# Performance work log

Measured on AMD Instinct MI355X. Metric: run time of the kernel, lower is better.

## Reference

```python
import jax, jax.numpy as jnp
import numpy as np
import math

THETA = 10000.0
D_K = 128
MAX_SEQ_LEN = 4096
BATCH, HEADS, SEQ = 4, 16, 2048


def _build_rope(theta, d_k, max_seq_len):
    # Faithful to the torch loop: rope[s, 2i, 2i]=cos, rope[s, 2i, 2i+1]=sin,
    # rope[s, 2i+1, 2i]=-sin, rope[s, 2i+1, 2i+1]=cos, with t = s / theta**(2i/d_k)
    pos = jnp.arange(max_seq_len, dtype=jnp.float32)  # [S]
    i = jnp.arange(d_k // 2, dtype=jnp.float32)       # [d/2]
    inv_freq = theta ** (-(2.0 * i) / d_k)            # [d/2]
    t = pos[:, None] * inv_freq[None, :]              # [S, d/2]
    cos, sin = jnp.cos(t), jnp.sin(t)
    even = 2 * jnp.arange(d_k // 2)
    odd = even + 1
    rope = jnp.zeros((max_seq_len, d_k, d_k), dtype=jnp.float32)
    rope = rope.at[:, even, even].set(cos)
    rope = rope.at[:, even, odd].set(sin)
    rope = rope.at[:, odd, even].set(-sin)
    rope = rope.at[:, odd, odd].set(cos)
    return rope


def setup_inputs() -> dict:
    key = jax.random.key(0)
    kx, kp = jax.random.split(key)
    x = jax.random.normal(kx, (BATCH, HEADS, SEQ, D_K), dtype=jnp.float32)
    token_positions = jax.random.randint(kp, (SEQ,), 0, SEQ, dtype=jnp.int64) if jax.config.jax_enable_x64 else jax.random.randint(kp, (SEQ,), 0, SEQ, dtype=jnp.int32)
    rope = _build_rope(THETA, D_K, MAX_SEQ_LEN)
    return {"x": x, "rope": rope, "token_positions": token_positions}


def reference(x, rope, token_positions):
    seq_len = x.shape[-2]
    # original: transpose(-2,-3), einsum '... s b d, s d e -> ... s b e', transpose back.
    # Equivalent single einsum with x in [..., h, s, d] layout:
    result = jnp.einsum('...hsd,sde->...hse', x, rope[:seq_len])
    # gather along the seq axis (-2) with token_positions (after rotation, as in source)
    return result[..., token_positions, :]
```

## Files before the change

kernel.cpp:

```cpp
#include <hip/hip_runtime.h>


#define SEQL 2048
#define DK   128
#define NBH  64

__global__ __launch_bounds__(256) void rope_gather_kernel(
        const float* __restrict__ x,
        const float* __restrict__ rope,
        const int* __restrict__ tp,
        float* __restrict__ out) {
    const int s = blockIdx.x;
    const int p = tp[s];
    const int q = threadIdx.x & 31;
    const int g = threadIdx.x >> 5;

    const float* rp = rope + (size_t)p * (DK * DK);
    const int i0 = q << 1;
    const float2 cs0 = *reinterpret_cast<const float2*>(rp + (size_t)258 * i0);
    const float2 cs1 = *reinterpret_cast<const float2*>(rp + (size_t)258 * (i0 + 1));

    const size_t rowstride = (size_t)SEQL * DK;
    const size_t xbase = (size_t)p * DK + (q << 2);
    const size_t obase = (size_t)s * DK + (q << 2);

    #pragma unroll
    for (int bh = g; bh < NBH; bh += 8) {
        const float4 xv = *reinterpret_cast<const float4*>(x + xbase + (size_t)bh * rowstride);
        float4 o;
        o.x = xv.x * cs0.x - xv.y * cs0.y;
        o.y = xv.x * cs0.y + xv.y * cs0.x;
        o.z = xv.z * cs1.x - xv.w * cs1.y;
        o.w = xv.z * cs1.y + xv.w * cs1.x;
        *reinterpret_cast<float4*>(out + obase + (size_t)bh * rowstride) = o;
    }
}

extern "C" void kernel_launch(void* const* d_in, const int* in_sizes, int n_in,
                              void* d_out, int out_size, void* d_ws, size_t ws_size,
                              hipStream_t stream) {
    const float* x    = (const float*)d_in[0];
    const float* rope = (const float*)d_in[1];
    const int*   tp   = (const int*)d_in[2];
    float*       out  = (float*)d_out;

    rope_gather_kernel<<<SEQL, 256, 0, stream>>>(x, rope, tp, out);
}
```

Measured before the change: 30.32 us.

## Replace gather with inverse-index scatter so each position is rotated once

Builds an inverse map from each source position to the output rows that reference it, using atomics into a workspace capped at 64 duplicates per position. A scatter kernel then reads and rotates each distinct x row once and writes it to every output row that maps to it. Positions no token refers to are skipped entirely. The aim is to cut redundant x reads, since the random positions contain duplicates. The cost is a memset, an extra kernel launch and uneven work across blocks. Positions repeated more than 64 times would silently produce wrong output.

```diff
diff --git a/kernel.cpp b/kernel.cpp
--- a/kernel.cpp
+++ b/kernel.cpp
@@ -4,6 +4,66 @@
 #define SEQL 2048
 #define DK   128
 #define NBH  64
+#define KCAP 64
+
+__global__ void build_inverse_kernel(const int* __restrict__ tp,
+                                     int* __restrict__ counts,
+                                     int* __restrict__ lists) {
+    int s = blockIdx.x * blockDim.x + threadIdx.x;
+    if (s >= SEQL) return;
+    int p = tp[s];
+    int slot = atomicAdd(&counts[p], 1);
+    if (slot < KCAP) lists[p * KCAP + slot] = s;
+}
+
+__global__ __launch_bounds__(256) void rope_scatter_kernel(
+        const float* __restrict__ x,
+        const float* __restrict__ rope,
+        float* __restrict__ out,
+        const int* __restrict__ counts,
+        const int* __restrict__ lists) {
+    const int p = blockIdx.x;
+    const int cnt = counts[p];
+    if (cnt == 0) return;
+
+    const int q = threadIdx.x & 31;
+    const int g = threadIdx.x >> 5;
+
+    const float* rp = rope + (size_t)p * (DK * DK);
+    const int i0 = q << 1;
+    const float2 cs0 = *reinterpret_cast<const float2*>(rp + (size_t)258 * i0);
+    const float2 cs1 = *reinterpret_cast<const float2*>(rp + (size_t)258 * (i0 + 1));
+
+    const size_t slice = (size_t)SEQL * DK;
+    const size_t xq = (size_t)p * DK + (q << 2);
+
+    float4 o0, o1, o2, o3, o4, o5, o6, o7;
+    {
+        float4 xv;
+        #define ROT(T, BH) \
+            xv = *reinterpret_cast<const float4*>(x + (size_t)(BH) * slice + xq); \
+            T.x = xv.x * cs0.x - xv.y * cs0.y; \
+            T.y = xv.x * cs0.y + xv.y * cs0.x; \
+            T.z = xv.z * cs1.x - xv.w * cs1.y; \
+            T.w = xv.z * cs1.y + xv.w * cs1.x;
+        ROT(o0, g +  0) ROT(o1, g +  8) ROT(o2, g + 16) ROT(o3, g + 24)
+        ROT(o4, g + 32) ROT(o5, g + 40) ROT(o6, g + 48) ROT(o7, g + 56)
+        #undef ROT
+    }
+
+    for (int j = 0; j < cnt; ++j) {
+        const int s = lists[p * KCAP + j];
+        float* ob = out + (size_t)s * DK + (q << 2);
+        *reinterpret_cast<float4*>(ob + (size_t)(g +  0) * slice) = o0;
+        *reinterpret_cast<float4*>(ob + (size_t)(g +  8) * slice) = o1;
+        *reinterpret_cast<float4*>(ob + (size_t)(g + 16) * slice) = o2;
+        *reinterpret_cast<float4*>(ob + (size_t)(g + 24) * slice) = o3;
+        *reinterpret_cast<float4*>(ob + (size_t)(g + 32) * slice) = o4;
+        *reinterpret_cast<float4*>(ob + (size_t)(g + 40) * slice) = o5;
+        *reinterpret_cast<float4*>(ob + (size_t)(g + 48) * slice) = o6;
+        *reinterpret_cast<float4*>(ob + (size_t)(g + 56) * slice) = o7;
+    }
+}
 
 __global__ __launch_bounds__(256) void rope_gather_kernel(
         const float* __restrict__ x,
@@ -44,5 +104,17 @@
     const int*   tp   = (const int*)d_in[2];
     float*       out  = (float*)d_out;
 
-    rope_gather_kernel<<<SEQL, 256, 0, stream>>>(x, rope, tp, out);
+    const size_t need = (size_t)SEQL * sizeof(int)
+                      + (size_t)SEQL * KCAP * sizeof(int);
+    if (ws_size < need) {
+        rope_gather_kernel<<<SEQL, 256, 0, stream>>>(x, rope, tp, out);
+        return;
+    }
+
+    int* counts = (int*)d_ws;
+    int* lists  = counts + SEQL;
+
+    hipMemsetAsync(counts, 0, SEQL * sizeof(int), stream);
+    build_inverse_kernel<<<SEQL / 256, 256, 0, stream>>>(tp, counts, lists);
+    rope_scatter_kernel<<<SEQL, 256, 0, stream>>>(x, rope, out, counts, lists);
 }
```

After: 32.69 us. +7.8%, slower.

## Precompute gathered cos/sin table and flatten rope output writes with nontemporal stores

Applied to the files above, without the earlier changes.

Adds a pre-pass kernel that gathers the cos/sin pairs for each token position into a compact workspace table. The main kernel then maps threads over a flat output index so that each block writes contiguous output, and it uses nontemporal stores. The aim is to cut scattered reads of the large rope tensor and make the store pattern friendlier. The cost is an extra kernel launch and a workspace round trip, and the code falls back to the old kernel when the workspace is too small.

```diff
diff --git a/kernel.cpp b/kernel.cpp
--- a/kernel.cpp
+++ b/kernel.cpp
@@ -4,6 +4,51 @@
 #define SEQL 2048
 #define DK   128
 #define NBH  64
+#define BLK  256
+#define NBLK 2048
+#define ITER 8
+
+typedef float vfloat4 __attribute__((ext_vector_type(4)));
+
+__global__ void build_cs_kernel(const float* __restrict__ rope,
+                                const int* __restrict__ tp,
+                                float2* __restrict__ cstab) {
+    int t = blockIdx.x * blockDim.x + threadIdx.x;
+    int s = t >> 6, i = t & 63;
+    int p = tp[s];
+    cstab[t] = *reinterpret_cast<const float2*>(rope + (size_t)p * (DK * DK) + (size_t)258 * i);
+}
+
+__global__ __launch_bounds__(BLK) void rope_flat_kernel(
+        const float* __restrict__ x,
+        const float2* __restrict__ cstab,
+        const int* __restrict__ tp,
+        float* __restrict__ out) {
+    const int idx0 = blockIdx.x * BLK + threadIdx.x;
+    const int row0 = idx0 >> 5;
+    const int q    = idx0 & 31;
+    const int s    = row0 & (SEQL - 1);
+    const int bh0  = row0 >> 11;
+    const int p    = tp[s];
+
+    const float4 cs = *reinterpret_cast<const float4*>(cstab + (size_t)s * 64 + (q << 1));
+
+    const size_t slice = (size_t)SEQL * DK;
+    const float* xb = x + (size_t)p * DK + (q << 2);
+    float* ob = out + (size_t)idx0 * 4;
+    const size_t ostep = (size_t)NBLK * BLK * 4;
+
+    #pragma unroll
+    for (int k = 0; k < ITER; ++k) {
+        const float4 xv = *reinterpret_cast<const float4*>(xb + (size_t)(bh0 + 8 * k) * slice);
+        vfloat4 o;
+        o.x = xv.x * cs.x - xv.y * cs.y;
+        o.y = xv.x * cs.y + xv.y * cs.x;
+        o.z = xv.z * cs.z - xv.w * cs.w;
+        o.w = xv.z * cs.w + xv.w * cs.z;
+        __builtin_nontemporal_store(o, reinterpret_cast<vfloat4*>(ob + (size_t)k * ostep));
+    }
+}
 
 __global__ __launch_bounds__(256) void rope_gather_kernel(
         const float* __restrict__ x,
@@ -44,5 +89,13 @@
     const int*   tp   = (const int*)d_in[2];
     float*       out  = (float*)d_out;
 
-    rope_gather_kernel<<<SEQL, 256, 0, stream>>>(x, rope, tp, out);
+    const size_t need = (size_t)SEQL * (DK / 2) * sizeof(float2);
+    if (ws_size < need) {
+        rope_gather_kernel<<<SEQL, 256, 0, stream>>>(x, rope, tp, out);
+        return;
+    }
+
+    float2* cstab = (float2*)d_ws;
+    build_cs_kernel<<<SEQL * (DK / 2) / 256, 256, 0, stream>>>(rope, tp, cstab);
+    rope_flat_kernel<<<NBLK, BLK, 0, stream>>>(x, cstab, tp, out);
 }
```

Result: slower. 31.10 us (+2.6%).
